# Optimization experiments

Measured on AMD Instinct MI355X. Metric: run time of the kernel, lower is better.

The kernel has to match this reference:

```python
import jax, jax.numpy as jnp
import numpy as np

EMBED_DIM = 1024
NUM_HEADS = 16
HEAD_DIM = EMBED_DIM // NUM_HEADS
B, S = 4, 2048


def setup_inputs() -> dict:
    key = jax.random.key(0)
    k1, k2, k3, k4, k5 = jax.random.split(key, 5)
    x = jax.random.normal(k1, (B, S, EMBED_DIM), dtype=jnp.float32)
    # torch nn.Linear params: W [out, in], b [out]; init scale ~ 1/sqrt(in)
    s = 1.0 / np.sqrt(EMBED_DIM)
    qkv_w = jax.random.uniform(k2, (3 * EMBED_DIM, EMBED_DIM), jnp.float32, -s, s)
    qkv_b = jax.random.uniform(k3, (3 * EMBED_DIM,), jnp.float32, -s, s)
    out_w = jax.random.uniform(k4, (EMBED_DIM, EMBED_DIM), jnp.float32, -s, s)
    out_b = jax.random.uniform(k5, (EMBED_DIM,), jnp.float32, -s, s)
    return {"x": x, "qkv_w": qkv_w, "qkv_b": qkv_b, "out_w": out_w, "out_b": out_b}


def reference(x, qkv_w, qkv_b, out_w, out_b):
    b, s, e = x.shape
    # qkv: [B,S,3E]
    qkv = x @ qkv_w.T + qkv_b
    # Faithful to source: reshape to [B,S,H,3*hd] then transpose -> [B,H,S,3*hd]
    qkv = qkv.reshape(b, s, NUM_HEADS, 3 * HEAD_DIM).transpose(0, 2, 1, 3)
    q, k, v = jnp.split(qkv, 3, axis=-1)  # each [B,H,S,hd]
    q = q / np.sqrt(HEAD_DIM).astype(np.float32)
    scores = jnp.einsum('bhqd,bhkd->bhqk', q, k)  # [B,H,S,S]
    attn = jax.nn.softmax(scores, axis=-1)
    out = jnp.einsum('bhqk,bhkd->bhqd', attn, v)  # [B,H,S,hd]
    out = out.transpose(0, 2, 1, 3).reshape(b, s, e)
    return out @ out_w.T + out_b
```

## Files before the change

kernel.cpp:

```cpp
#include <hip/hip_runtime.h>

#define EMBED   1024
#define THREE_E 3072
#define NHEAD   16
#define HDIM    64
#define BATCH   4
#define SEQ     2048
#define MTOK    (BATCH * SEQ)
#define QKW     2048

typedef __attribute__((ext_vector_type(8))) _Float16 half8;
typedef __attribute__((ext_vector_type(4))) _Float16 half4;
typedef __attribute__((ext_vector_type(4))) float    f32x4;

#define QSCALE 0.18033688011112042f

__device__ inline f32x4 mfma16(half8 a, half8 b, f32x4 c) {
    return __builtin_amdgcn_mfma_f32_16x16x32_f16(a, b, c, 0, 0, 0);
}
__device__ inline f32x4 mfma16k16(half4 a, half4 b, f32x4 c) {
    return __builtin_amdgcn_mfma_f32_16x16x16f16(a, b, c, 0, 0, 0);
}

__device__ inline float exp2x(float x) {
    float r;
    asm("v_exp_f32 %0, %1" : "=v"(r) : "v"(x));
    return r;
}

__device__ inline void gld16(const void* g, void* l) {
    __builtin_amdgcn_global_load_lds(
        (const __attribute__((address_space(1))) unsigned*)g,
        (__attribute__((address_space(3))) unsigned*)l, 16, 0, 0);
}

__global__ __launch_bounds__(256) void tohi3_kernel(
    const float* __restrict__ x,  _Float16* __restrict__ xo,
    const float* __restrict__ w1, _Float16* __restrict__ w1o,
    const float* __restrict__ w2, _Float16* __restrict__ w2o)
{
    const int bid = blockIdx.x;
    const float* src; _Float16* dst; int base;
    if (bid < 8192)             { src = x;  dst = xo;  base = bid * 1024; }
    else if (bid < 8192 + 3072) { src = w1; dst = w1o; base = (bid - 8192) * 1024; }
    else                        { src = w2; dst = w2o; base = (bid - 11264) * 1024; }
    const int i = base + (threadIdx.x << 2);
    const float4 v = *(const float4*)(src + i);
    half4 h;
    h[0] = (_Float16)v.x; h[1] = (_Float16)v.y;
    h[2] = (_Float16)v.z; h[3] = (_Float16)v.w;
    *(half4*)(dst + i) = h;
}

template<int OMODE>
__global__ __launch_bounds__(512, 2) void gemm_big(
    const _Float16* __restrict__ Ahi,
    const _Float16* __restrict__ Bhi,
    const float*  __restrict__ bias,
    float* __restrict__ Cf,
    _Float16* __restrict__ QKhi,
    _Float16* __restrict__ Vthi,
    int N, int K)
{
    __shared__ __align__(16) _Float16 sA[2][8][2][64][8];
    __shared__ __align__(16) _Float16 sB[2][16][2][64][8];

    const int tid  = threadIdx.x;
    const int w    = tid >> 6;
    const int lane = tid & 63;
    const int quad = lane >> 4;
    const int c    = lane & 15;
    const int wr   = w >> 2, wc = w & 3;

    const int gx   = gridDim.x;
    const int nwg  = gx * gridDim.y;
    const int lin0 = blockIdx.y * gx + blockIdx.x;
    const int wg   = (lin0 & 7) * (nwg >> 3) + (lin0 >> 3);
    const int m0   = (wg / gx) << 7;
    const int n0   = (wg % gx) << 8;

    f32x4 acc[4][4];
#pragma unroll
    for (int i = 0; i < 4; ++i)
#pragma unroll
        for (int j = 0; j < 4; ++j) acc[i][j] = (f32x4){0.f, 0.f, 0.f, 0.f};

    const int rg0 = w >> 1, ksb = w & 1;
    const size_t sK64 = (size_t)64 * K;
    const _Float16* ap = Ahi + (size_t)(m0 + rg0 * 16 + c) * K + ksb * 32 + quad * 8;
    const _Float16* bp = Bhi + (size_t)(n0 + rg0 * 16 + c) * K + ksb * 32 + quad * 8;

    gld16(ap,            &sA[0][rg0][ksb][0][0]);
    gld16(ap + sK64,     &sA[0][4 + rg0][ksb][0][0]);
    gld16(bp,            &sB[0][rg0][ksb][0][0]);
    gld16(bp + sK64,     &sB[0][4 + rg0][ksb][0][0]);
    gld16(bp + 2 * sK64, &sB[0][8 + rg0][ksb][0][0]);
    gld16(bp + 3 * sK64, &sB[0][12 + rg0][ksb][0][0]);
    ap += 64; bp += 64;

    const int NT = K >> 6;
    for (int t = 0; t < NT; ++t) {
        const int slot = t & 1;
        asm volatile("s_waitcnt vmcnt(0)" ::: "memory");
        asm volatile("s_barrier" ::: "memory");
        const bool pre = (t + 1) < NT;

        half8 aH[4][2], bH[4][2];
#pragma unroll
        for (int fr = 0; fr < 4; ++fr)
#pragma unroll
            for (int ks = 0; ks < 2; ++ks)
                aH[fr][ks] = *(const half8*)&sA[slot][wr * 4 + fr][ks][lane][0];
#pragma unroll
        for (int fc = 0; fc < 2; ++fc)
#pragma unroll
            for (int ks = 0; ks < 2; ++ks)
                bH[fc][ks] = *(const half8*)&sB[slot][wc * 4 + fc][ks][lane][0];
        if (pre) {
            gld16(ap,        &sA[slot ^ 1][rg0][ksb][0][0]);
            gld16(ap + sK64, &sA[slot ^ 1][4 + rg0][ksb][0][0]);
            gld16(bp,        &sB[slot ^ 1][rg0][ksb][0][0]);
        }
        __builtin_amdgcn_s_setprio(1);
#pragma unroll
        for (int fr = 0; fr < 4; ++fr)
#pragma unroll
            for (int fc = 0; fc < 2; ++fc)
#pragma unroll
                for (int ks = 0; ks < 2; ++ks)
                    acc[fr][fc] = mfma16(aH[fr][ks], bH[fc][ks], acc[fr][fc]);
        __builtin_amdgcn_s_setprio(0);
        asm volatile("s_barrier" ::: "memory");

#pragma unroll
        for (int fc = 2; fc < 4; ++fc)
#pragma unroll
            for (int ks = 0; ks < 2; ++ks)
                bH[fc][ks] = *(const half8*)&sB[slot][wc * 4 + fc][ks][lane][0];
        if (pre) {
            gld16(bp + sK64,     &sB[slot ^ 1][4 + rg0][ksb][0][0]);
            gld16(bp + 2 * sK64, &sB[slot ^ 1][8 + rg0][ksb][0][0]);
            gld16(bp + 3 * sK64, &sB[slot ^ 1][12 + rg0][ksb][0][0]);
            ap += 64; bp += 64;
        }
        __builtin_amdgcn_s_setprio(1);
#pragma unroll
        for (int fr = 0; fr < 4; ++fr)
#pragma unroll
            for (int fc = 2; fc < 4; ++fc)
#pragma unroll
                for (int ks = 0; ks < 2; ++ks)
                    acc[fr][fc] = mfma16(aH[fr][ks], bH[fc][ks], acc[fr][fc]);
        __builtin_amdgcn_s_setprio(0);
    }

#pragma unroll
    for (int fc = 0; fc < 4; ++fc) {
        const int n  = n0 + wc * 64 + fc * 16 + c;
        const float bb = bias[n];
        const int h  = n / 192;
        const int rem = n - h * 192;
#pragma unroll
        for (int fr = 0; fr < 4; ++fr) {
            const int mb = m0 + wr * 64 + fr * 16 + (quad << 2);
            if constexpr (OMODE == 0) {
#pragma unroll
                for (int r = 0; r < 4; ++r)
                    Cf[(size_t)(mb + r) * N + n] = acc[fr][fc][r] + bb;
            } else {
                if (rem < 128) {
                    const size_t col = h * 128 + rem;
                    const float scale = (rem < 64) ? QSCALE : 1.0f;
#pragma unroll
                    for (int r = 0; r < 4; ++r)
                        QKhi[(size_t)(mb + r) * QKW + col] =
                            (_Float16)((acc[fr][fc][r] + bb) * scale);
                } else {
                    const int d = rem - 128;
                    const int b = mb >> 11;
                    const int s = mb & 2047;
                    half4 h4;
#pragma unroll
                    for (int r = 0; r < 4; ++r)
                        h4[r] = (_Float16)(acc[fr][fc][r] + bb);
                    const size_t off = ((size_t)(h * 64 + d) * BATCH + b) * SEQ + s;
                    *(half4*)(Vthi + off) = h4;
                }
            }
        }
    }
}

__global__ __launch_bounds__(256, 4) void attn_mfma(
    const _Float16* __restrict__ qkhi,
    const _Float16* __restrict__ vthi,
    _Float16* __restrict__ attnf)
{
    __shared__ __align__(16) _Float16 Kf[2][8][512];
    __shared__ __align__(16) _Float16 Vf[2][8][512];

    const int tid  = threadIdx.x;
    const int w    = tid >> 6;
    const int lane = tid & 63;
    const int quad = lane >> 4;
    const int c    = lane & 15;

    const int lin = blockIdx.x;
    const int g   = lin & 7;
    const int s   = lin >> 3;
    const int bh  = g * 8 + (s >> 4);
    const int qt  = s & 15;
    const int b   = bh >> 4, h = bh & 15;
    const int q0  = qt * 128;

    const size_t bSEQ  = (size_t)b * SEQ;
    const int    qcol  = h * 128;
    const int    kcol  = h * 128 + 64;
    const size_t vbase = ((size_t)(h * 64) * BATCH + b) * SEQ;

    half8 qh[2][2];
#pragma unroll
    for (int t = 0; t < 2; ++t) {
        const size_t row = (bSEQ + q0 + w * 32 + t * 16 + c) * QKW;
#pragma unroll
        for (int ks = 0; ks < 2; ++ks)
            qh[t][ks] = *(const half8*)(qkhi + row + qcol + ks * 32 + quad * 8);
    }

    f32x4 lacc[2];
    f32x4 oacc[4][2];
#pragma unroll
    for (int t = 0; t < 2; ++t) {
        lacc[t] = (f32x4){0.f, 0.f, 0.f, 0.f};
#pragma unroll
        for (int v = 0; v < 4; ++v) oacc[v][t] = (f32x4){0.f, 0.f, 0.f, 0.f};
    }

    const half4 one4 = {(_Float16)1.f, (_Float16)1.f, (_Float16)1.f, (_Float16)1.f};

    const int ku0 = w >> 1,       kks0 = w & 1;
    const int ku1 = (4 + w) >> 1, kks1 = (4 + w) & 1;
    const _Float16* kp0 = qkhi + (bSEQ + ku0 * 16 + c) * QKW + kcol + kks0 * 32 + quad * 8;
    const _Float16* kp1 = qkhi + (bSEQ + ku1 * 16 + c) * QKW + kcol + kks1 * 32 + quad * 8;
    const int lswz = lane ^ ((((lane >> 3) & 1) << 1) | (((lane >> 4) & 1) << 2));
    const int qs   = lswz >> 4, cs = lswz & 15;
    const _Float16* vp0 = vthi + vbase + (size_t)(ku0 * 16 + cs) * (BATCH * SEQ) + kks0 * 32 + qs * 8;
    const _Float16* vp1 = vthi + vbase + (size_t)(ku1 * 16 + cs) * (BATCH * SEQ) + kks1 * 32 + qs * 8;

    auto stageKV = [&](int bfs) {
        gld16(kp0, &Kf[bfs][w][0]);
        gld16(kp1, &Kf[bfs][4 + w][0]);
        gld16(vp0, &Vf[bfs][w][0]);
        gld16(vp1, &Vf[bfs][4 + w][0]);
        kp0 += 64 * QKW; kp1 += 64 * QKW; vp0 += 64; vp1 += 64;
    };

    stageKV(0);
    int bf = 0;

    for (int kt = 0; kt < SEQ / 64; ++kt) {
        __syncthreads();
        if (kt + 1 < SEQ / 64) stageKV(bf ^ 1);

        f32x4 sacc[2][4];
        __builtin_amdgcn_s_setprio(1);
#pragma unroll
        for (int u = 0; u < 4; ++u) {
            const half8 kh0 = *(const half8*)&Kf[bf][(u << 1) + 0][lane << 3];
            const half8 kh1 = *(const half8*)&Kf[bf][(u << 1) + 1][lane << 3];
#pragma unroll
            for (int t = 0; t < 2; ++t) {
                f32x4 a = (f32x4){0.f, 0.f, 0.f, 0.f};
                a = mfma16(kh0, qh[t][0], a);
                a = mfma16(kh1, qh[t][1], a);
                sacc[t][u] = a;
            }
        }
        __builtin_amdgcn_s_setprio(0);

        half4 pk[2][4];
#pragma unroll
        for (int t = 0; t < 2; ++t)
#pragma unroll
            for (int u = 0; u < 4; ++u) {
                const float p0 = exp2x(sacc[t][u][0]);
                const float p1 = exp2x(sacc[t][u][1]);
                const float p2 = exp2x(sacc[t][u][2]);
                const float p3 = exp2x(sacc[t][u][3]);
                const auto lo = __builtin_amdgcn_cvt_pkrtz(p0, p1);
                const auto hi = __builtin_amdgcn_cvt_pkrtz(p2, p3);
                half4 pp;
                pp[0] = (_Float16)lo[0]; pp[1] = (_Float16)lo[1];
                pp[2] = (_Float16)hi[0]; pp[3] = (_Float16)hi[1];
                pk[t][u] = pp;
            }

        half4 va[4][4];
#pragma unroll
        for (int v = 0; v < 4; ++v)
#pragma unroll
            for (int u = 0; u < 4; ++u) {
                const int qp   = ((u & 1) << 1) + (quad >> 1);
                int elem = ((qp << 4) + c) * 8 + ((quad & 1) << 2);
                elem ^= (((c >> 3) & 1) << 4) ^ ((qp & 1) << 5);
                va[v][u] = *(const half4*)&Vf[bf][(v << 1) + (u >> 1)][elem];
            }

        __builtin_amdgcn_s_setprio(1);
#pragma unroll
        for (int t = 0; t < 2; ++t) {
#pragma unroll
            for (int v = 0; v < 4; ++v) {
                f32x4 a = oacc[v][t];
#pragma unroll
                for (int u = 0; u < 4; ++u)
                    a = mfma16k16(va[v][u], pk[t][u], a);
                oacc[v][t] = a;
            }
            f32x4 l = lacc[t];
#pragma unroll
            for (int u = 0; u < 4; ++u)
                l = mfma16k16(one4, pk[t][u], l);
            lacc[t] = l;
        }
        __builtin_amdgcn_s_setprio(0);

        bf ^= 1;
    }

#pragma unroll
    for (int t = 0; t < 2; ++t) {
        const float inv = 1.0f / lacc[t][0];
        const int tok = q0 + w * 32 + t * 16 + c;
#pragma unroll
        for (int v = 0; v < 4; ++v) {
            half4 o;
#pragma unroll
            for (int r = 0; r < 4; ++r) o[r] = (_Float16)(oacc[v][t][r] * inv);
            *(half4*)&attnf[(bSEQ + tok) * EMBED + h * HDIM + v * 16 + (quad << 2)] = o;
        }
    }
}

extern "C" void kernel_launch(void* const* d_in, const int* in_sizes, int n_in,
                              void* d_out, int out_size, void* d_ws, size_t ws_size,
                              hipStream_t stream)
{
    const float* x     = (const float*)d_in[0];
    const float* qkv_w = (const float*)d_in[1];
    const float* qkv_b = (const float*)d_in[2];
    const float* out_w = (const float*)d_in[3];
    const float* out_b = (const float*)d_in[4];

    _Float16* qkhi  = (_Float16*)d_ws;
    _Float16* vthi  = qkhi  + (size_t)MTOK * QKW;
    _Float16* w1hi  = vthi  + (size_t)NHEAD * HDIM * BATCH * SEQ;
    _Float16* w2hi  = w1hi  + (size_t)THREE_E * EMBED;
    _Float16* attnf = w2hi  + (size_t)EMBED * EMBED;

    _Float16* xhi = (_Float16*)d_out;

    tohi3_kernel<<<dim3(12288), 256, 0, stream>>>(x, xhi, qkv_w, w1hi, out_w, w2hi);

    gemm_big<1><<<dim3(THREE_E / 256, MTOK / 128), 512, 0, stream>>>(
        xhi, w1hi, qkv_b, nullptr, qkhi, vthi, THREE_E, EMBED);

    attn_mfma<<<dim3(1024), 256, 0, stream>>>(qkhi, vthi, attnf);

    gemm_big<0><<<dim3(EMBED / 256, MTOK / 128), 512, 0, stream>>>(
        attnf, w2hi, out_b, (float*)d_out, nullptr, nullptr, EMBED, EMBED);
}
```

Measured before the change: 316.1 us.

## Triple-buffer LDS in big GEMM to prefetch two K-tiles ahead

Grows the shared-memory staging buffers in the projection GEMM from two slots to three and issues global-to-LDS loads two K-tiles ahead. The per-iteration wait becomes a partial vmcnt(6) instead of a full drain, so loads for the following tile can stay in flight across the barrier. The goal is to hide global memory latency better. The cost is 50% more LDS per block, which could limit the two-blocks-per-CU occupancy requested by the launch bounds.

```diff
diff --git a/kernel.cpp b/kernel.cpp
--- a/kernel.cpp
+++ b/kernel.cpp
@@ -62,8 +62,8 @@
     _Float16* __restrict__ Vthi,
     int N, int K)
 {
-    __shared__ __align__(16) _Float16 sA[2][8][2][64][8];
-    __shared__ __align__(16) _Float16 sB[2][16][2][64][8];
+    __shared__ __align__(16) _Float16 sA[3][8][2][64][8];
+    __shared__ __align__(16) _Float16 sB[3][16][2][64][8];
 
     const int tid  = threadIdx.x;
     const int w    = tid >> 6;
@@ -90,20 +90,30 @@
     const _Float16* ap = Ahi + (size_t)(m0 + rg0 * 16 + c) * K + ksb * 32 + quad * 8;
     const _Float16* bp = Bhi + (size_t)(n0 + rg0 * 16 + c) * K + ksb * 32 + quad * 8;
 
-    gld16(ap,            &sA[0][rg0][ksb][0][0]);
-    gld16(ap + sK64,     &sA[0][4 + rg0][ksb][0][0]);
-    gld16(bp,            &sB[0][rg0][ksb][0][0]);
-    gld16(bp + sK64,     &sB[0][4 + rg0][ksb][0][0]);
-    gld16(bp + 2 * sK64, &sB[0][8 + rg0][ksb][0][0]);
-    gld16(bp + 3 * sK64, &sB[0][12 + rg0][ksb][0][0]);
-    ap += 64; bp += 64;
+    auto stage_p0 = [&](int sl) {
+        gld16(ap,            &sA[sl][rg0][ksb][0][0]);
+        gld16(ap + sK64,     &sA[sl][4 + rg0][ksb][0][0]);
+        gld16(bp,            &sB[sl][rg0][ksb][0][0]);
+    };
+    auto stage_p1 = [&](int sl) {
+        gld16(bp + sK64,     &sB[sl][4 + rg0][ksb][0][0]);
+        gld16(bp + 2 * sK64, &sB[sl][8 + rg0][ksb][0][0]);
+        gld16(bp + 3 * sK64, &sB[sl][12 + rg0][ksb][0][0]);
+        ap += 64; bp += 64;
+    };
+
+    stage_p0(0); stage_p1(0);
+    stage_p0(1); stage_p1(1);
 
     const int NT = K >> 6;
+    int slot = 0;
     for (int t = 0; t < NT; ++t) {
-        const int slot = t & 1;
-        asm volatile("s_waitcnt vmcnt(0)" ::: "memory");
-        asm volatile("s_barrier" ::: "memory");
-        const bool pre = (t + 1) < NT;
+        if (t + 1 < NT) { asm volatile("s_waitcnt vmcnt(6)" ::: "memory"); }
+        else            { asm volatile("s_waitcnt vmcnt(0)" ::: "memory"); }
+        __builtin_amdgcn_s_barrier();
+
+        const bool pre = (t + 2) < NT;
+        int ns = slot + 2; if (ns >= 3) ns -= 3;
 
         half8 aH[4][2], bH[4][2];
 #pragma unroll
@@ -116,11 +126,7 @@
 #pragma unroll
             for (int ks = 0; ks < 2; ++ks)
                 bH[fc][ks] = *(const half8*)&sB[slot][wc * 4 + fc][ks][lane][0];
-        if (pre) {
-            gld16(ap,        &sA[slot ^ 1][rg0][ksb][0][0]);
-            gld16(ap + sK64, &sA[slot ^ 1][4 + rg0][ksb][0][0]);
-            gld16(bp,        &sB[slot ^ 1][rg0][ksb][0][0]);
-        }
+        if (pre) stage_p0(ns);
         __builtin_amdgcn_s_setprio(1);
 #pragma unroll
         for (int fr = 0; fr < 4; ++fr)
@@ -130,19 +136,14 @@
                 for (int ks = 0; ks < 2; ++ks)
                     acc[fr][fc] = mfma16(aH[fr][ks], bH[fc][ks], acc[fr][fc]);
         __builtin_amdgcn_s_setprio(0);
-        asm volatile("s_barrier" ::: "memory");
+        __builtin_amdgcn_s_barrier();
 
 #pragma unroll
         for (int fc = 2; fc < 4; ++fc)
 #pragma unroll
             for (int ks = 0; ks < 2; ++ks)
                 bH[fc][ks] = *(const half8*)&sB[slot][wc * 4 + fc][ks][lane][0];
-        if (pre) {
-            gld16(bp + sK64,     &sB[slot ^ 1][4 + rg0][ksb][0][0]);
-            gld16(bp + 2 * sK64, &sB[slot ^ 1][8 + rg0][ksb][0][0]);
-            gld16(bp + 3 * sK64, &sB[slot ^ 1][12 + rg0][ksb][0][0]);
-            ap += 64; bp += 64;
-        }
+        if (pre) stage_p1(ns);
         __builtin_amdgcn_s_setprio(1);
 #pragma unroll
         for (int fr = 0; fr < 4; ++fr)
@@ -152,6 +153,8 @@
                 for (int ks = 0; ks < 2; ++ks)
                     acc[fr][fc] = mfma16(aH[fr][ks], bH[fc][ks], acc[fr][fc]);
         __builtin_amdgcn_s_setprio(0);
+
+        slot = (slot == 2) ? 0 : slot + 1;
     }
 
 #pragma unroll
```

Result: faster. 295.6 us (-6.5%).
